# Kernel optimization log

Hardware: AMD Instinct MI355X
Metric: run time of the kernel (lower is better)

Reference implementation:

```python
import jax, jax.numpy as jnp
import numpy as np


def setup_inputs() -> dict:
    key = jax.random.key(0)
    g, s, d = 4, 4096, 2048
    inp = jax.random.normal(key, (g, s, d), dtype=jnp.float32)
    return {"input": inp, "num_experts": 16}


def reference(input, num_experts):
    g, s, _ = input.shape
    assert s % num_experts == 0
    capacity = 2 * s // num_experts
    tok = jnp.arange(s)
    expert = tok % num_experts          # [s]
    slot = tok // num_experts           # [s]
    # one vectorized scatter instead of the per-token python loop
    out = jnp.zeros((g, s, num_experts, capacity), dtype=input.dtype)
    out = out.at[:, tok, expert, slot].set(1.0)
    return (0.0, out, out.astype(bool))
```

## Files before the change

### kernel.cpp

```cpp
#include <hip/hip_runtime.h>

#define TENSOR_ELEMS 134217728LL
#define TOTAL_ELEMS  268435457LL
#define N_FLOAT4     67108864LL

__global__ void rrg_fill_zero(float4* __restrict__ out4, long long n4) {
    long long i = (long long)blockIdx.x * blockDim.x + threadIdx.x;
    const long long stride = (long long)gridDim.x * blockDim.x;
    const float4 z = make_float4(0.f, 0.f, 0.f, 0.f);
    for (; i < n4; i += stride) {
        out4[i] = z;
    }
    if (blockIdx.x == 0 && threadIdx.x == 0) {
        ((float*)out4)[TOTAL_ELEMS - 1] = 0.0f;
    }
}

__global__ void rrg_set_ones(float* __restrict__ out) {
    const int t = blockIdx.x * blockDim.x + threadIdx.x;
    const int tok  = t & 4095;
    const int e    = tok & 15;
    const int slot = tok >> 4;
    const long long idx = (((long long)t * 16) + e) * 512 + slot;
    out[1 + idx] = 1.0f;
    out[1 + TENSOR_ELEMS + idx] = 1.0f;
}

extern "C" void kernel_launch(void* const* d_in, const int* in_sizes, int n_in,
                              void* d_out, int out_size, void* d_ws, size_t ws_size,
                              hipStream_t stream) {
    (void)d_in; (void)in_sizes; (void)n_in; (void)d_ws; (void)ws_size;
    float* out = (float*)d_out;

    rrg_fill_zero<<<8192, 256, 0, stream>>>((float4*)out, N_FLOAT4);

    rrg_set_ones<<<16384 / 256, 256, 0, stream>>>(out);
}
```

Baseline: 1.147 ms.

## Fuse zero-fill and one-hot scatter into a single computed-value write kernel

Replaces the zero-fill kernel plus the separate scatter kernel with one kernel. Each thread computes the one-hot value of its four output elements from the index arithmetic and writes a single float4. This removes the second launch and the scattered stores, and uses one thread per float4 instead of a grid-stride loop. In exchange every element needs a few integer ops, and the grid becomes very large (262144 blocks).

```diff
diff --git a/kernel.cpp b/kernel.cpp
--- a/kernel.cpp
+++ b/kernel.cpp
@@ -1,38 +1,35 @@
 #include <hip/hip_runtime.h>
+
 
 #define TENSOR_ELEMS 134217728LL
 #define TOTAL_ELEMS  268435457LL
-#define N_FLOAT4     67108864LL
+#define N_FLOAT4     67108864
 
-__global__ void rrg_fill_zero(float4* __restrict__ out4, long long n4) {
-    long long i = (long long)blockIdx.x * blockDim.x + threadIdx.x;
-    const long long stride = (long long)gridDim.x * blockDim.x;
-    const float4 z = make_float4(0.f, 0.f, 0.f, 0.f);
-    for (; i < n4; i += stride) {
-        out4[i] = z;
+__global__ void __launch_bounds__(256) rrg_write(float4* __restrict__ out4) {
+    const int i = blockIdx.x * 256 + threadIdx.x;
+    float4 v = make_float4(0.f, 0.f, 0.f, 0.f);
+    const long long n0 = 4LL * i;
+#pragma unroll
+    for (int j = 0; j < 4; ++j) {
+        const long long n = n0 + j;
+        if (n >= 1) {
+            long long a = n - 1;
+            if (a >= TENSOR_ELEMS) a -= TENSOR_ELEMS;
+            const int slot = (int)(a & 511);
+            const int e    = (int)((a >> 9) & 15);
+            const int tok  = (int)((a >> 13) & 4095);
+            if (e == (tok & 15) && slot == (tok >> 4))
+                (&v.x)[j] = 1.0f;
+        }
     }
-    if (blockIdx.x == 0 && threadIdx.x == 0) {
+    out4[i] = v;
+    if (i == 0)
         ((float*)out4)[TOTAL_ELEMS - 1] = 0.0f;
-    }
-}
-
-__global__ void rrg_set_ones(float* __restrict__ out) {
-    const int t = blockIdx.x * blockDim.x + threadIdx.x;
-    const int tok  = t & 4095;
-    const int e    = tok & 15;
-    const int slot = tok >> 4;
-    const long long idx = (((long long)t * 16) + e) * 512 + slot;
-    out[1 + idx] = 1.0f;
-    out[1 + TENSOR_ELEMS + idx] = 1.0f;
 }
 
 extern "C" void kernel_launch(void* const* d_in, const int* in_sizes, int n_in,
                               void* d_out, int out_size, void* d_ws, size_t ws_size,
                               hipStream_t stream) {
     (void)d_in; (void)in_sizes; (void)n_in; (void)d_ws; (void)ws_size;
-    float* out = (float*)d_out;
-
-    rrg_fill_zero<<<8192, 256, 0, stream>>>((float4*)out, N_FLOAT4);
-
-    rrg_set_ones<<<16384 / 256, 256, 0, stream>>>(out);
+    rrg_write<<<N_FLOAT4 / 256, 256, 0, stream>>>((float4*)d_out);
 }
```

Measured after the change: 1.056 ms, median of 2. 1.09x faster.
